# Kernel tuning notes

Hardware: AMD Instinct MI355X
Metric: run time of the kernel (lower is better)

The kernel has to match this reference:

```python
import jax, jax.numpy as jnp
import numpy as np

N, K, D, V = 20000, 16, 256, 64  # nodes, neighbors, embed_dim, edge vocab


def setup_inputs() -> dict:
    key = jax.random.key(0)
    ks = jax.random.split(key, 16)
    s = 1.0 / np.sqrt(2 * D)  # Linear(512 -> 256) init scale
    return {
        "node_reps": jax.random.normal(ks[0], (1, N, D), jnp.float32),
        "in_indices": jax.random.randint(ks[1], (1, N, K), 0, N, jnp.int32),
        "in_edges": jax.random.randint(ks[2], (1, N, K), 0, V, jnp.int32),
        "in_mask": jax.random.uniform(ks[3], (1, N, K), jnp.float32),
        "out_indices": jax.random.randint(ks[4], (1, N, K), 0, N, jnp.int32),
        "out_edges": jax.random.randint(ks[5], (1, N, K), 0, V, jnp.int32),
        "out_mask": jax.random.uniform(ks[6], (1, N, K), jnp.float32),
        "edge_emb_1": jax.random.normal(ks[7], (V, D), jnp.float32),
        "W_1": jax.random.uniform(ks[8], (2 * D, D), jnp.float32, -s, s),
        "b_1": jnp.zeros((D,), jnp.float32),
        "edge_emb_2": jax.random.normal(ks[9], (V, D), jnp.float32),
        "W_2": jax.random.uniform(ks[10], (2 * D, D), jnp.float32, -s, s),
        "b_2": jnp.zeros((D,), jnp.float32),
        "edge_emb_3": jax.random.normal(ks[11], (V, D), jnp.float32),
        "W_3": jax.random.uniform(ks[12], (2 * D, D), jnp.float32, -s, s),
        "b_3": jnp.zeros((D,), jnp.float32),
    }


def gcn_layer(node_reps, in_idx, in_edg, in_msk, out_idx, out_edg, out_msk,
              edge_emb, W, b):
    # node_reps: [1, N, D]; dropout is identity in eval mode.
    nodes = node_reps[0]  # [N, D]; batch_size == 1 as in the original repo

    def agg(idx, edg, msk):
        nbr = nodes[idx]          # gather: [1, N, K, D]
        erep = edge_emb[edg]      # embedding lookup: [1, N, K, D]
        reps = jnp.concatenate([nbr, erep], axis=3) * msk[..., None]
        return reps.sum(axis=2)   # masked sum over neighbors: [1, N, 2D]

    in_reps = agg(in_idx, in_edg, in_msk)
    out_reps = agg(out_idx, out_edg, out_msk)
    in_nodes = in_reps[0] @ W + b    # [N, D]
    out_nodes = out_reps[0] @ W + b  # [N, D]
    return node_reps + out_nodes + in_nodes  # broadcast -> [1, N, D]


def reference(node_reps, in_indices, in_edges, in_mask,
              out_indices, out_edges, out_mask,
              edge_emb_1, W_1, b_1, edge_emb_2, W_2, b_2, edge_emb_3, W_3, b_3):
    nbrs = (in_indices, in_edges, in_mask, out_indices, out_edges, out_mask)
    hidden = gcn_layer(node_reps, *nbrs, edge_emb_1, W_1, b_1)  # gc1
    mu = gcn_layer(hidden, *nbrs, edge_emb_2, W_2, b_2)          # gc2
    logvar = gcn_layer(hidden, *nbrs, edge_emb_3, W_3, b_3)      # gc3

    mu_t = jnp.tanh(mu[0])        # [N, D]
    lv_t = jnp.tanh(logvar[0])    # [N, D]
    n_nodes = mu_t.shape[0]
    kld = (-0.5 / n_nodes) * jnp.mean(
        jnp.sum(1.0 + 2.0 * lv_t - mu_t ** 2 - jnp.exp(lv_t) ** 2, axis=1))
    return hidden, kld
```

## Files before the change

kernel.cpp:

```cpp
#include <hip/hip_runtime.h>
#include <math.h>

#define NN 20000
#define KK 16
#define DD 256
#define VV 64
#define NT1 16

typedef __attribute__((ext_vector_type(8))) __bf16 bf16x8;
typedef __attribute__((ext_vector_type(4))) float floatx4;
typedef __attribute__((ext_vector_type(2))) float floatx2;
typedef __attribute__((ext_vector_type(8))) unsigned short ushort8;

__device__ __forceinline__ float4 ld4(const float* p) { return *reinterpret_cast<const float4*>(p); }

__device__ __forceinline__ unsigned short f2bf(float f) {
    union { float f; unsigned u; } v; v.f = f;
    unsigned r = v.u + 0x7FFFu + ((v.u >> 16) & 1u);
    return (unsigned short)(r >> 16);
}
__device__ __forceinline__ float bf2f(unsigned short u) {
    union { unsigned u; float f; } v; v.u = ((unsigned)u) << 16;
    return v.f;
}
__device__ __forceinline__ unsigned char f2q(float f) {
    return (unsigned char)(__builtin_amdgcn_cvt_pk_fp8_f32(f, 0.f, 0u, false) & 0xFFu);
}
__device__ __forceinline__ float q2f(unsigned char q) {
    floatx2 r = __builtin_amdgcn_cvt_pk_f32_fp8((unsigned)q, false);
    return r.x;
}
__device__ __forceinline__ float ftanh(float v) {
    float e = __expf(2.f * v);
    return 1.f - 2.f * __builtin_amdgcn_rcpf(e + 1.f);
}

__global__ __launch_bounds__(256) void ewk3(const float* __restrict__ e1, const float* __restrict__ W1,
                                            const float* __restrict__ e2, const float* __restrict__ W2,
                                            const float* __restrict__ e3, const float* __restrict__ W3,
                                            float* __restrict__ EW) {
    int layer = blockIdx.y;
    const float* emb = layer == 0 ? e1 : (layer == 1 ? e2 : e3);
    const float* W   = layer == 0 ? W1 : (layer == 1 ? W2 : W3);
    int v = blockIdx.x, d = threadIdx.x;
    float acc = 0.f;
    #pragma unroll 8
    for (int j = 0; j < 256; ++j)
        acc += emb[v * DD + j] * W[(size_t)(256 + j) * DD + d];
    EW[(size_t)layer * VV * DD + v * DD + d] = acc;
}

__global__ __launch_bounds__(256) void packU2(const float* __restrict__ W1, const float* __restrict__ EW1,
                                              const float* __restrict__ W2, const float* __restrict__ EW2,
                                              const float* __restrict__ W3, const float* __restrict__ EW3,
                                              unsigned short* __restrict__ U1, unsigned short* __restrict__ U23) {
    int blk = blockIdx.x;
    int NT; unsigned short* U; const float *Wa, *EWa, *Wb, *EWb; int g;
    if (blk < 40) { NT = 16; U = U1;  Wa = W1; EWa = EW1; Wb = W1; EWb = EW1; g = blk * 256 + threadIdx.x; }
    else          { NT = 32; U = U23; Wa = W2; EWa = EW2; Wb = W3; EWb = EW3; g = (blk - 40) * 256 + threadIdx.x; }
    int lane = g & 63, ntk = g >> 6;
    int nt = ntk % NT, kt = ntk / NT;
    if (kt >= 10) return;
    int n = nt * 16 + (lane & 15);
    int kbase = kt * 32 + (lane >> 4) * 8;
    const float* W = Wa; const float* EW = EWa;
    if (n >= 256) { W = Wb; EW = EWb; n -= 256; }
    unsigned short o8[8];
    #pragma unroll
    for (int j = 0; j < 8; ++j) {
        int k = kbase + j;
        float v = (k < 256) ? W[(size_t)k * DD + n] : EW[(size_t)(k - 256) * DD + n];
        o8[j] = f2bf(v);
    }
    *reinterpret_cast<uint4*>(&U[(size_t)g * 8]) = *reinterpret_cast<uint4*>(o8);
}

__global__ __launch_bounds__(256) void prep(const int* __restrict__ ie, const float* __restrict__ im,
                                            const int* __restrict__ oe, const float* __restrict__ om,
                                            const float* __restrict__ x,
                                            unsigned short* __restrict__ Hc, unsigned short* __restrict__ xh) {
    int w = threadIdx.x >> 6, lane = threadIdx.x & 63;
    int n = blockIdx.x * 4 + w;
    int e = 0; float m = 0.f;
    if (lane < 16)      { e = ie[n * KK + lane];      m = im[n * KK + lane]; }
    else if (lane < 32) { e = oe[n * KK + lane - 16]; m = om[n * KK + lane - 16]; }
    float h = 0.f;
    #pragma unroll
    for (int j = 0; j < 32; ++j) {
        int ev = __shfl(e, j);
        float mv = __shfl(m, j);
        if (ev == lane) h += mv;
    }
    Hc[(size_t)n * 64 + lane] = f2bf(h);
    size_t base = (size_t)blockIdx.x * 1024 + threadIdx.x * 4;
    float4 v = ld4(x + base);
    ushort4 o; o.x = f2bf(v.x); o.y = f2bf(v.y); o.z = f2bf(v.z); o.w = f2bf(v.w);
    *reinterpret_cast<ushort4*>(xh + base) = o;
}

__global__ __launch_bounds__(256) void fmm1(const unsigned short* __restrict__ xh, const unsigned short* __restrict__ Hc,
                                            const int* __restrict__ ii, const float* __restrict__ im,
                                            const int* __restrict__ oi, const float* __restrict__ om,
                                            const unsigned short* __restrict__ U, const float* __restrict__ b,
                                            float* __restrict__ out, unsigned char* __restrict__ h8) {
    __shared__ unsigned short sA[16 * 336];
    __shared__ int sidx[16][32];
    __shared__ float smsk[16][32];
    int n0 = blockIdx.x * 16;
    int tid = threadIdx.x;
    for (int q = tid; q < 512; q += 256) {
        int r = q >> 5, j = q & 31;
        int n = n0 + r;
        sidx[r][j] = (j < 16) ? ii[n * KK + j] : oi[n * KK + j - 16];
        smsk[r][j] = (j < 16) ? im[n * KK + j] : om[n * KK + j - 16];
    }
    if (tid < 128) {
        int r = tid >> 3, k8 = tid & 7;
        *reinterpret_cast<uint4*>(&sA[r * 336 + 256 + k8 * 8]) =
            *reinterpret_cast<const uint4*>(&Hc[(size_t)(n0 + r) * 64 + k8 * 8]);
    }
    __syncthreads();
    int lane = tid & 63, w = tid >> 6;
    int half = lane >> 5, c = (lane & 31) * 8;
    #pragma unroll
    for (int rr = 0; rr < 4; ++rr) {
        int row = w * 4 + rr;
        float acc[8] = {0.f, 0.f, 0.f, 0.f, 0.f, 0.f, 0.f, 0.f};
        #pragma unroll
        for (int j = 0; j < 16; ++j) {
            int j2 = j * 2 + half;
            int idx = sidx[row][j2];
            float m = smsk[row][j2];
            ushort8 u = *reinterpret_cast<const ushort8*>(xh + (size_t)idx * DD + c);
            #pragma unroll
            for (int z = 0; z < 8; ++z) acc[z] += m * bf2f(u[z]);
        }
        #pragma unroll
        for (int z = 0; z < 8; ++z) acc[z] += __shfl_xor(acc[z], 32);
        if (half == 0) {
            unsigned short o8[8];
            #pragma unroll
            for (int z = 0; z < 8; ++z) o8[z] = f2bf(acc[z]);
            *reinterpret_cast<uint4*>(&sA[row * 336 + c]) = *reinterpret_cast<uint4*>(o8);
        }
    }
    __syncthreads();
    int lr = lane & 15, quad = lane >> 4;
    float xp[4][4], bb[4];
    #pragma unroll
    for (int t = 0; t < 4; ++t) {
        int col = (w * 4 + t) * 16 + lr;
        bb[t] = 2.f * b[col];
        #pragma unroll
        for (int r = 0; r < 4; ++r)
            xp[t][r] = bf2f(xh[(size_t)(n0 + quad * 4 + r) * DD + col]);
    }
    floatx4 z = {0.f, 0.f, 0.f, 0.f};
    floatx4 acc[4] = {z, z, z, z};
    for (int kt = 0; kt < 10; ++kt) {
        bf16x8 a = *reinterpret_cast<const bf16x8*>(&sA[lr * 336 + kt * 32 + quad * 8]);
        #pragma unroll
        for (int t = 0; t < 4; ++t) {
            bf16x8 bf = *reinterpret_cast<const bf16x8*>(&U[(size_t)((kt * NT1 + w * 4 + t) * 64 + lane) * 8]);
            acc[t] = __builtin_amdgcn_mfma_f32_16x16x32_bf16(a, bf, acc[t], 0, 0, 0);
        }
    }
    #pragma unroll
    for (int t = 0; t < 4; ++t) {
        int col = (w * 4 + t) * 16 + lr;
        #pragma unroll
        for (int r = 0; r < 4; ++r) {
            size_t o = (size_t)(n0 + quad * 4 + r) * DD + col;
            float v = xp[t][r] + bb[t] + acc[t][r];
            out[o] = v;
            h8[o] = f2q(v);
        }
    }
}

__global__ __launch_bounds__(256) void fmm23(const unsigned char* __restrict__ h8, const unsigned short* __restrict__ Hc,
                                             const int* __restrict__ ii, const float* __restrict__ im,
                                             const int* __restrict__ oi, const float* __restrict__ om,
                                             const unsigned short* __restrict__ U, const float* __restrict__ b2,
                                             const float* __restrict__ b3, float* __restrict__ partials) {
    __shared__ unsigned short sA[16 * 336];
    __shared__ int sidx[16][32];
    __shared__ float smsk[16][32];
    __shared__ float red[4];
    int n0 = blockIdx.x * 16;
    int tid = threadIdx.x;
    for (int q = tid; q < 512; q += 256) {
        int r = q >> 5, j = q & 31;
        int n = n0 + r;
        sidx[r][j] = (j < 16) ? ii[n * KK + j] : oi[n * KK + j - 16];
        smsk[r][j] = (j < 16) ? im[n * KK + j] : om[n * KK + j - 16];
    }
    if (tid < 128) {
        int r = tid >> 3, k8 = tid & 7;
        *reinterpret_cast<uint4*>(&sA[r * 336 + 256 + k8 * 8]) =
            *reinterpret_cast<const uint4*>(&Hc[(size_t)(n0 + r) * 64 + k8 * 8]);
    }
    __syncthreads();
    int lane = tid & 63, w = tid >> 6;
    int g = lane >> 4, cl = lane & 15;
    #pragma unroll
    for (int rr = 0; rr < 4; ++rr) {
        int row = w * 4 + rr;
        float acc[16];
        #pragma unroll
        for (int z = 0; z < 16; ++z) acc[z] = 0.f;
        #pragma unroll
        for (int j = 0; j < 8; ++j) {
            int r = g * 8 + j;
            int idx = sidx[row][r];
            float m = smsk[row][r];
            uint4 u = *reinterpret_cast<const uint4*>(h8 + (size_t)idx * DD + cl * 16);
            unsigned dw[4] = {u.x, u.y, u.z, u.w};
            #pragma unroll
            for (int d = 0; d < 4; ++d) {
                floatx2 f01 = __builtin_amdgcn_cvt_pk_f32_fp8(dw[d], false);
                floatx2 f23 = __builtin_amdgcn_cvt_pk_f32_fp8(dw[d], true);
                acc[d * 4 + 0] += m * f01.x; acc[d * 4 + 1] += m * f01.y;
                acc[d * 4 + 2] += m * f23.x; acc[d * 4 + 3] += m * f23.y;
            }
        }
        #pragma unroll
        for (int z = 0; z < 16; ++z) {
            acc[z] += __shfl_xor(acc[z], 16);
            acc[z] += __shfl_xor(acc[z], 32);
        }
        if (g == 0) {
            unsigned short o16[16];
            #pragma unroll
            for (int z = 0; z < 16; ++z) o16[z] = f2bf(acc[z]);
            uint4* dst = reinterpret_cast<uint4*>(&sA[row * 336 + cl * 16]);
            dst[0] = reinterpret_cast<uint4*>(o16)[0];
            dst[1] = reinterpret_cast<uint4*>(o16)[1];
        }
    }
    __syncthreads();
    int lr = lane & 15, quad = lane >> 4;
    float hp[4][4], bm[4], bl[4];
    #pragma unroll
    for (int t = 0; t < 4; ++t) {
        int col = (w * 4 + t) * 16 + lr;
        bm[t] = 2.f * b2[col];
        bl[t] = 2.f * b3[col];
        #pragma unroll
        for (int r = 0; r < 4; ++r)
            hp[t][r] = q2f(h8[(size_t)(n0 + quad * 4 + r) * DD + col]);
    }
    floatx4 z = {0.f, 0.f, 0.f, 0.f};
    floatx4 am[4] = {z, z, z, z};
    floatx4 al[4] = {z, z, z, z};
    for (int kt = 0; kt < 10; ++kt) {
        bf16x8 a = *reinterpret_cast<const bf16x8*>(&sA[lr * 336 + kt * 32 + quad * 8]);
        #pragma unroll
        for (int t = 0; t < 4; ++t) {
            int nt = w * 4 + t;
            bf16x8 bmu = *reinterpret_cast<const bf16x8*>(&U[(size_t)((kt * 32 + nt) * 64 + lane) * 8]);
            bf16x8 blv = *reinterpret_cast<const bf16x8*>(&U[(size_t)((kt * 32 + 16 + nt) * 64 + lane) * 8]);
            am[t] = __builtin_amdgcn_mfma_f32_16x16x32_bf16(a, bmu, am[t], 0, 0, 0);
            al[t] = __builtin_amdgcn_mfma_f32_16x16x32_bf16(a, blv, al[t], 0, 0, 0);
        }
    }
    float kacc = 0.f;
    #pragma unroll
    for (int t = 0; t < 4; ++t) {
        #pragma unroll
        for (int r = 0; r < 4; ++r) {
            float h = hp[t][r];
            float tm = ftanh(h + bm[t] + am[t][r]);
            float tl = ftanh(h + bl[t] + al[t][r]);
            kacc += (1.f - tm * tm) + (2.f * tl - __expf(2.f * tl));
        }
    }
    #pragma unroll
    for (int off = 32; off > 0; off >>= 1) kacc += __shfl_xor(kacc, off);
    if (lane == 0) red[w] = kacc;
    __syncthreads();
    if (tid == 0)
        partials[blockIdx.x] = red[0] + red[1] + red[2] + red[3];
}

__global__ __launch_bounds__(256) void kred(const float* __restrict__ partials, int np,
                                            float* __restrict__ out) {
    __shared__ double red[256];
    double l = 0.0;
    for (int i = threadIdx.x; i < np; i += 256) l += (double)partials[i];
    red[threadIdx.x] = l;
    __syncthreads();
    for (int s = 128; s > 0; s >>= 1) {
        if (threadIdx.x < s) red[threadIdx.x] += red[threadIdx.x + s];
        __syncthreads();
    }
    if (threadIdx.x == 0)
        out[0] = (float)(red[0] * (-0.5 / ((double)NN * (double)NN)));
}

extern "C" void kernel_launch(void* const* d_in, const int* in_sizes, int n_in,
                              void* d_out, int out_size, void* d_ws, size_t ws_size,
                              hipStream_t stream) {
    const float* x  = (const float*)d_in[0];
    const int*   ii = (const int*)d_in[1];
    const int*   ie = (const int*)d_in[2];
    const float* im = (const float*)d_in[3];
    const int*   oi = (const int*)d_in[4];
    const int*   oe = (const int*)d_in[5];
    const float* om = (const float*)d_in[6];
    const float* e1 = (const float*)d_in[7];
    const float* W1 = (const float*)d_in[8];
    const float* b1 = (const float*)d_in[9];
    const float* e2 = (const float*)d_in[10];
    const float* W2 = (const float*)d_in[11];
    const float* b2 = (const float*)d_in[12];
    const float* e3 = (const float*)d_in[13];
    const float* W3 = (const float*)d_in[14];
    const float* b3 = (const float*)d_in[15];
    float* out = (float*)d_out;

    char* ws = (char*)d_ws;
    float*          EW    = (float*)(ws);
    unsigned short* U1    = (unsigned short*)(ws + 196608);
    unsigned short* U23   = (unsigned short*)(ws + 360448);
    float*          parts = (float*)(ws + 688128);
    unsigned short* Hc    = (unsigned short*)(ws + 696128);
    unsigned short* xh    = (unsigned short*)(ws + 3256128);
    unsigned char*  h8    = (unsigned char*)(ws + 13496128);

    ewk3  <<<dim3(VV, 3), 256, 0, stream>>>(e1, W1, e2, W2, e3, W3, EW);
    packU2<<<120, 256, 0, stream>>>(W1, EW, W2, EW + VV * DD, W3, EW + 2 * VV * DD, U1, U23);
    prep  <<<NN / 4, 256, 0, stream>>>(ie, im, oe, om, x, Hc, xh);
    fmm1  <<<NN / 16, 256, 0, stream>>>(xh, Hc, ii, im, oi, om, U1, b1, out, h8);
    fmm23 <<<NN / 16, 256, 0, stream>>>(h8, Hc, ii, im, oi, om, U23, b2, b3, parts);
    kred  <<<1, 256, 0, stream>>>(parts, NN / 16, out + (size_t)NN * DD);
}
```

Measured before the change: 223.8 us.

## Remap gather so each thread owns a row slice over all neighbors

Reorganizes the neighbor-gather phase in both fused kernels so each thread accumulates a 16-column slice of one node over all 32 neighbors. This removes the cross-lane shuffle reductions and the per-row loop. Residual and bias loads are hoisted before the gather to overlap their latency, the LDS row stride is padded from 336 to 352, and launch bounds request 4 blocks per CU. The trade-off is that each thread now issues more serial dependent loads (32 neighbors, unrolled by 8), and the occupancy hint may cap registers and cause spills.

After: 244.5 us. 1.09x slower.

```diff
diff --git a/kernel.cpp b/kernel.cpp
--- a/kernel.cpp
+++ b/kernel.cpp
@@ -6,6 +6,7 @@
 #define DD 256
 #define VV 64
 #define NT1 16
+#define SAS 352
 
 typedef __attribute__((ext_vector_type(8))) __bf16 bf16x8;
 typedef __attribute__((ext_vector_type(4))) float floatx4;
@@ -98,12 +99,12 @@
     *reinterpret_cast<ushort4*>(xh + base) = o;
 }
 
-__global__ __launch_bounds__(256) void fmm1(const unsigned short* __restrict__ xh, const unsigned short* __restrict__ Hc,
-                                            const int* __restrict__ ii, const float* __restrict__ im,
-                                            const int* __restrict__ oi, const float* __restrict__ om,
-                                            const unsigned short* __restrict__ U, const float* __restrict__ b,
-                                            float* __restrict__ out, unsigned char* __restrict__ h8) {
-    __shared__ unsigned short sA[16 * 336];
+__global__ __launch_bounds__(256, 4) void fmm1(const unsigned short* __restrict__ xh, const unsigned short* __restrict__ Hc,
+                                               const int* __restrict__ ii, const float* __restrict__ im,
+                                               const int* __restrict__ oi, const float* __restrict__ om,
+                                               const unsigned short* __restrict__ U, const float* __restrict__ b,
+                                               float* __restrict__ out, unsigned char* __restrict__ h8) {
+    __shared__ unsigned short sA[16 * SAS];
     __shared__ int sidx[16][32];
     __shared__ float smsk[16][32];
     int n0 = blockIdx.x * 16;
@@ -116,35 +117,10 @@
     }
     if (tid < 128) {
         int r = tid >> 3, k8 = tid & 7;
-        *reinterpret_cast<uint4*>(&sA[r * 336 + 256 + k8 * 8]) =
+        *reinterpret_cast<uint4*>(&sA[r * SAS + 256 + k8 * 8]) =
             *reinterpret_cast<const uint4*>(&Hc[(size_t)(n0 + r) * 64 + k8 * 8]);
     }
-    __syncthreads();
     int lane = tid & 63, w = tid >> 6;
-    int half = lane >> 5, c = (lane & 31) * 8;
-    #pragma unroll
-    for (int rr = 0; rr < 4; ++rr) {
-        int row = w * 4 + rr;
-        float acc[8] = {0.f, 0.f, 0.f, 0.f, 0.f, 0.f, 0.f, 0.f};
-        #pragma unroll
-        for (int j = 0; j < 16; ++j) {
-            int j2 = j * 2 + half;
-            int idx = sidx[row][j2];
-            float m = smsk[row][j2];
-            ushort8 u = *reinterpret_cast<const ushort8*>(xh + (size_t)idx * DD + c);
-            #pragma unroll
-            for (int z = 0; z < 8; ++z) acc[z] += m * bf2f(u[z]);
-        }
-        #pragma unroll
-        for (int z = 0; z < 8; ++z) acc[z] += __shfl_xor(acc[z], 32);
-        if (half == 0) {
-            unsigned short o8[8];
-            #pragma unroll
-            for (int z = 0; z < 8; ++z) o8[z] = f2bf(acc[z]);
-            *reinterpret_cast<uint4*>(&sA[row * 336 + c]) = *reinterpret_cast<uint4*>(o8);
-        }
-    }
-    __syncthreads();
     int lr = lane & 15, quad = lane >> 4;
     float xp[4][4], bb[4];
     #pragma unroll
@@ -155,10 +131,38 @@
         for (int r = 0; r < 4; ++r)
             xp[t][r] = bf2f(xh[(size_t)(n0 + quad * 4 + r) * DD + col]);
     }
+    __syncthreads();
+    {
+        int gr = tid >> 4, gc = tid & 15;
+        float acc[16];
+        #pragma unroll
+        for (int z = 0; z < 16; ++z) acc[z] = 0.f;
+        const unsigned short* basecol = xh + gc * 16;
+        #pragma unroll 8
+        for (int j = 0; j < 32; ++j) {
+            int idx = sidx[gr][j];
+            float m = smsk[gr][j];
+            const unsigned short* p = basecol + (size_t)idx * DD;
+            ushort8 u0 = *reinterpret_cast<const ushort8*>(p);
+            ushort8 u1 = *reinterpret_cast<const ushort8*>(p + 8);
+            #pragma unroll
+            for (int z = 0; z < 8; ++z) {
+                acc[z]     += m * bf2f(u0[z]);
+                acc[z + 8] += m * bf2f(u1[z]);
+            }
+        }
+        unsigned short o16[16];
+        #pragma unroll
+        for (int z = 0; z < 16; ++z) o16[z] = f2bf(acc[z]);
+        uint4* dst = reinterpret_cast<uint4*>(&sA[gr * SAS + gc * 16]);
+        dst[0] = reinterpret_cast<uint4*>(o16)[0];
+        dst[1] = reinterpret_cast<uint4*>(o16)[1];
+    }
+    __syncthreads();
     floatx4 z = {0.f, 0.f, 0.f, 0.f};
     floatx4 acc[4] = {z, z, z, z};
     for (int kt = 0; kt < 10; ++kt) {
-        bf16x8 a = *reinterpret_cast<const bf16x8*>(&sA[lr * 336 + kt * 32 + quad * 8]);
+        bf16x8 a = *reinterpret_cast<const bf16x8*>(&sA[lr * SAS + kt * 32 + quad * 8]);
         #pragma unroll
         for (int t = 0; t < 4; ++t) {
             bf16x8 bf = *reinterpret_cast<const bf16x8*>(&U[(size_t)((kt * NT1 + w * 4 + t) * 64 + lane) * 8]);
@@ -178,12 +182,12 @@
     }
 }
 
-__global__ __launch_bounds__(256) void fmm23(const unsigned char* __restrict__ h8, const unsigned short* __restrict__ Hc,
-                                             const int* __restrict__ ii, const float* __restrict__ im,
-                                             const int* __restrict__ oi, const float* __restrict__ om,
-                                             const unsigned short* __restrict__ U, const float* __restrict__ b2,
-                                             const float* __restrict__ b3, float* __restrict__ partials) {
-    __shared__ unsigned short sA[16 * 336];
+__global__ __launch_bounds__(256, 4) void fmm23(const unsigned char* __restrict__ h8, const unsigned short* __restrict__ Hc,
+                                                const int* __restrict__ ii, const float* __restrict__ im,
+                                                const int* __restrict__ oi, const float* __restrict__ om,
+                                                const unsigned short* __restrict__ U, const float* __restrict__ b2,
+                                                const float* __restrict__ b3, float* __restrict__ partials) {
+    __shared__ unsigned short sA[16 * SAS];
     __shared__ int sidx[16][32];
     __shared__ float smsk[16][32];
     __shared__ float red[4];
@@ -197,24 +201,33 @@
     }
     if (tid < 128) {
         int r = tid >> 3, k8 = tid & 7;
-        *reinterpret_cast<uint4*>(&sA[r * 336 + 256 + k8 * 8]) =
+        *reinterpret_cast<uint4*>(&sA[r * SAS + 256 + k8 * 8]) =
             *reinterpret_cast<const uint4*>(&Hc[(size_t)(n0 + r) * 64 + k8 * 8]);
     }
-    __syncthreads();
     int lane = tid & 63, w = tid >> 6;
-    int g = lane >> 4, cl = lane & 15;
-    #pragma unroll
-    for (int rr = 0; rr < 4; ++rr) {
-        int row = w * 4 + rr;
+    int lr = lane & 15, quad = lane >> 4;
+    float hp[4][4], bm[4], bl[4];
+    #pragma unroll
+    for (int t = 0; t < 4; ++t) {
+        int col = (w * 4 + t) * 16 + lr;
+        bm[t] = 2.f * b2[col];
+        bl[t] = 2.f * b3[col];
+        #pragma unroll
+        for (int r = 0; r < 4; ++r)
+            hp[t][r] = q2f(h8[(size_t)(n0 + quad * 4 + r) * DD + col]);
+    }
+    __syncthreads();
+    {
+        int gr = tid >> 4, gc = tid & 15;
         float acc[16];
         #pragma unroll
         for (int z = 0; z < 16; ++z) acc[z] = 0.f;
-        #pragma unroll
-        for (int j = 0; j < 8; ++j) {
-            int r = g * 8 + j;
-            int idx = sidx[row][r];
-            float m = smsk[row][r];
-            uint4 u = *reinterpret_cast<const uint4*>(h8 + (size_t)idx * DD + cl * 16);
+        const unsigned char* basecol = h8 + gc * 16;
+        #pragma unroll 8
+        for (int j = 0; j < 32; ++j) {
+            int idx = sidx[gr][j];
+            float m = smsk[gr][j];
+            uint4 u = *reinterpret_cast<const uint4*>(basecol + (size_t)idx * DD);
             unsigned dw[4] = {u.x, u.y, u.z, u.w};
             #pragma unroll
             for (int d = 0; d < 4; ++d) {
@@ -224,37 +237,19 @@
                 acc[d * 4 + 2] += m * f23.x; acc[d * 4 + 3] += m * f23.y;
             }
         }
-        #pragma unroll
-        for (int z = 0; z < 16; ++z) {
-            acc[z] += __shfl_xor(acc[z], 16);
-            acc[z] += __shfl_xor(acc[z], 32);
-        }
-        if (g == 0) {
-            unsigned short o16[16];
-            #pragma unroll
-            for (int z = 0; z < 16; ++z) o16[z] = f2bf(acc[z]);
-            uint4* dst = reinterpret_cast<uint4*>(&sA[row * 336 + cl * 16]);
-            dst[0] = reinterpret_cast<uint4*>(o16)[0];
-            dst[1] = reinterpret_cast<uint4*>(o16)[1];
-        }
-    }
-    __syncthreads();
-    int lr = lane & 15, quad = lane >> 4;
-    float hp[4][4], bm[4], bl[4];
-    #pragma unroll
-    for (int t = 0; t < 4; ++t) {
-        int col = (w * 4 + t) * 16 + lr;
-        bm[t] = 2.f * b2[col];
-        bl[t] = 2.f * b3[col];
-        #pragma unroll
-        for (int r = 0; r < 4; ++r)
-            hp[t][r] = q2f(h8[(size_t)(n0 + quad * 4 + r) * DD + col]);
-    }
+        unsigned short o16[16];
+        #pragma unroll
+        for (int z = 0; z < 16; ++z) o16[z] = f2bf(acc[z]);
+        uint4* dst = reinterpret_cast<uint4*>(&sA[gr * SAS + gc * 16]);
+        dst[0] = reinterpret_cast<uint4*>(o16)[0];
+        dst[1] = reinterpret_cast<uint4*>(o16)[1];
+    }
+    __syncthreads();
     floatx4 z = {0.f, 0.f, 0.f, 0.f};
     floatx4 am[4] = {z, z, z, z};
     floatx4 al[4] = {z, z, z, z};
     for (int kt = 0; kt < 10; ++kt) {
-        bf16x8 a = *reinterpret_cast<const bf16x8*>(&sA[lr * 336 + kt * 32 + quad * 8]);
+        bf16x8 a = *reinterpret_cast<const bf16x8*>(&sA[lr * SAS + kt * 32 + quad * 8]);
         #pragma unroll
         for (int t = 0; t < 4; ++t) {
             int nt = w * 4 + t;
```

## Fuse setup kernels, switch layers 2/3 matmul to FP8 MFMA, atomic KLD reduction

Applied to the files above, without the earlier changes.

Merges the edge-embedding projection, weight packing and prep into one setup launch, computing the EW rows inline inside the packing threads. Layers 2 and 3 now store weights, edge histograms and the aggregated A tile in FP8 and use the fp8 MFMA, which halves operand bytes and LDS traffic. The separate reduction kernel is replaced by a memset plus per-block float atomicAdd. This cuts launch count and memory traffic, but lowers numerical precision, makes the KLD sum order nondeterministic, and the fused EW computation is redundant across threads.

New measurement: 202.0 us. -9.7%, faster.

```diff
diff --git a/kernel.cpp b/kernel.cpp
--- a/kernel.cpp
+++ b/kernel.cpp
@@ -6,6 +6,8 @@
 #define DD 256
 #define VV 64
 #define NT1 16
+#define SAS 336
+#define SAS8 336
 
 typedef __attribute__((ext_vector_type(8))) __bf16 bf16x8;
 typedef __attribute__((ext_vector_type(4))) float floatx4;
@@ -35,67 +37,77 @@
     return 1.f - 2.f * __builtin_amdgcn_rcpf(e + 1.f);
 }
 
-__global__ __launch_bounds__(256) void ewk3(const float* __restrict__ e1, const float* __restrict__ W1,
-                                            const float* __restrict__ e2, const float* __restrict__ W2,
-                                            const float* __restrict__ e3, const float* __restrict__ W3,
-                                            float* __restrict__ EW) {
-    int layer = blockIdx.y;
-    const float* emb = layer == 0 ? e1 : (layer == 1 ? e2 : e3);
-    const float* W   = layer == 0 ? W1 : (layer == 1 ? W2 : W3);
-    int v = blockIdx.x, d = threadIdx.x;
-    float acc = 0.f;
-    #pragma unroll 8
-    for (int j = 0; j < 256; ++j)
-        acc += emb[v * DD + j] * W[(size_t)(256 + j) * DD + d];
-    EW[(size_t)layer * VV * DD + v * DD + d] = acc;
-}
-
-__global__ __launch_bounds__(256) void packU2(const float* __restrict__ W1, const float* __restrict__ EW1,
-                                              const float* __restrict__ W2, const float* __restrict__ EW2,
-                                              const float* __restrict__ W3, const float* __restrict__ EW3,
-                                              unsigned short* __restrict__ U1, unsigned short* __restrict__ U23) {
-    int blk = blockIdx.x;
-    int NT; unsigned short* U; const float *Wa, *EWa, *Wb, *EWb; int g;
-    if (blk < 40) { NT = 16; U = U1;  Wa = W1; EWa = EW1; Wb = W1; EWb = EW1; g = blk * 256 + threadIdx.x; }
-    else          { NT = 32; U = U23; Wa = W2; EWa = EW2; Wb = W3; EWb = EW3; g = (blk - 40) * 256 + threadIdx.x; }
-    int lane = g & 63, ntk = g >> 6;
-    int nt = ntk % NT, kt = ntk / NT;
-    if (kt >= 10) return;
-    int n = nt * 16 + (lane & 15);
-    int kbase = kt * 32 + (lane >> 4) * 8;
-    const float* W = Wa; const float* EW = EWa;
-    if (n >= 256) { W = Wb; EW = EWb; n -= 256; }
-    unsigned short o8[8];
-    #pragma unroll
-    for (int j = 0; j < 8; ++j) {
-        int k = kbase + j;
-        float v = (k < 256) ? W[(size_t)k * DD + n] : EW[(size_t)(k - 256) * DD + n];
-        o8[j] = f2bf(v);
-    }
-    *reinterpret_cast<uint4*>(&U[(size_t)g * 8]) = *reinterpret_cast<uint4*>(o8);
-}
-
-__global__ __launch_bounds__(256) void prep(const int* __restrict__ ie, const float* __restrict__ im,
-                                            const int* __restrict__ oe, const float* __restrict__ om,
-                                            const float* __restrict__ x,
-                                            unsigned short* __restrict__ Hc, unsigned short* __restrict__ xh) {
-    int w = threadIdx.x >> 6, lane = threadIdx.x & 63;
-    int n = blockIdx.x * 4 + w;
-    int e = 0; float m = 0.f;
-    if (lane < 16)      { e = ie[n * KK + lane];      m = im[n * KK + lane]; }
-    else if (lane < 32) { e = oe[n * KK + lane - 16]; m = om[n * KK + lane - 16]; }
-    float h = 0.f;
-    #pragma unroll
-    for (int j = 0; j < 32; ++j) {
-        int ev = __shfl(e, j);
-        float mv = __shfl(m, j);
-        if (ev == lane) h += mv;
-    }
-    Hc[(size_t)n * 64 + lane] = f2bf(h);
-    size_t base = (size_t)blockIdx.x * 1024 + threadIdx.x * 4;
-    float4 v = ld4(x + base);
-    ushort4 o; o.x = f2bf(v.x); o.y = f2bf(v.y); o.z = f2bf(v.z); o.w = f2bf(v.w);
-    *reinterpret_cast<ushort4*>(xh + base) = o;
+__global__ __launch_bounds__(256) void setup(
+    const int* __restrict__ ie, const float* __restrict__ im,
+    const int* __restrict__ oe, const float* __restrict__ om,
+    const float* __restrict__ x,
+    const float* __restrict__ e1, const float* __restrict__ W1,
+    const float* __restrict__ e2, const float* __restrict__ W2,
+    const float* __restrict__ e3, const float* __restrict__ W3,
+    unsigned short* __restrict__ U1, unsigned char* __restrict__ U23,
+    unsigned short* __restrict__ Hc, unsigned char* __restrict__ Hc8,
+    unsigned short* __restrict__ xh) {
+    int blk = blockIdx.x, tid = threadIdx.x;
+    if (blk < 120) {
+        int u1path = blk < 40;
+        int NT = u1path ? 16 : 32;
+        int g = (u1path ? blk : blk - 40) * 256 + tid;
+        int lane = g & 63, ntk = g >> 6;
+        int nt = ntk % NT, kt = ntk / NT;
+        if (kt >= 10) return;
+        int n = nt * 16 + (lane & 15);
+        int kbase = kt * 32 + (lane >> 4) * 8;
+        const float* W; const float* emb;
+        if (u1path)       { W = W1; emb = e1; }
+        else if (n < 256) { W = W2; emb = e2; }
+        else              { W = W3; emb = e3; n -= 256; }
+        float vals[8];
+        if (kbase < 256) {
+            #pragma unroll
+            for (int j = 0; j < 8; ++j) vals[j] = W[(size_t)(kbase + j) * DD + n];
+        } else {
+            int vb = kbase - 256;
+            #pragma unroll
+            for (int z = 0; z < 8; ++z) vals[z] = 0.f;
+            #pragma unroll 4
+            for (int j = 0; j < 256; ++j) {
+                float wv = W[(size_t)(256 + j) * DD + n];
+                #pragma unroll
+                for (int z = 0; z < 8; ++z) vals[z] += emb[(vb + z) * DD + j] * wv;
+            }
+        }
+        if (u1path) {
+            unsigned short o8[8];
+            #pragma unroll
+            for (int j = 0; j < 8; ++j) o8[j] = f2bf(vals[j]);
+            *reinterpret_cast<uint4*>(&U1[(size_t)g * 8]) = *reinterpret_cast<uint4*>(o8);
+        } else {
+            unsigned char o8[8];
+            #pragma unroll
+            for (int j = 0; j < 8; ++j) o8[j] = f2q(vals[j]);
+            *reinterpret_cast<uint2*>(&U23[(size_t)g * 8]) = *reinterpret_cast<uint2*>(o8);
+        }
+    } else {
+        int pb = blk - 120;
+        int w = tid >> 6, lane = tid & 63;
+        int n = pb * 4 + w;
+        int e = 0; float m = 0.f;
+        if (lane < 16)      { e = ie[n * KK + lane];      m = im[n * KK + lane]; }
+        else if (lane < 32) { e = oe[n * KK + lane - 16]; m = om[n * KK + lane - 16]; }
+        float h = 0.f;
+        #pragma unroll
+        for (int j = 0; j < 32; ++j) {
+            int ev = __shfl(e, j);
+            float mv = __shfl(m, j);
+            if (ev == lane) h += mv;
+        }
+        Hc [(size_t)n * 64 + lane] = f2bf(h);
+        Hc8[(size_t)n * 64 + lane] = f2q(h);
+        size_t base = (size_t)pb * 1024 + tid * 4;
+        float4 v = ld4(x + base);
+        ushort4 o; o.x = f2bf(v.x); o.y = f2bf(v.y); o.z = f2bf(v.z); o.w = f2bf(v.w);
+        *reinterpret_cast<ushort4*>(xh + base) = o;
+    }
 }
 
 __global__ __launch_bounds__(256) void fmm1(const unsigned short* __restrict__ xh, const unsigned short* __restrict__ Hc,
@@ -103,7 +115,7 @@
                                             const int* __restrict__ oi, const float* __restrict__ om,
                                             const unsigned short* __restrict__ U, const float* __restrict__ b,
                                             float* __restrict__ out, unsigned char* __restrict__ h8) {
-    __shared__ unsigned short sA[16 * 336];
+    __shared__ unsigned short sA[16 * SAS];
     __shared__ int sidx[16][32];
     __shared__ float smsk[16][32];
     int n0 = blockIdx.x * 16;
@@ -116,7 +128,7 @@
     }
     if (tid < 128) {
         int r = tid >> 3, k8 = tid & 7;
-        *reinterpret_cast<uint4*>(&sA[r * 336 + 256 + k8 * 8]) =
+        *reinterpret_cast<uint4*>(&sA[r * SAS + 256 + k8 * 8]) =
             *reinterpret_cast<const uint4*>(&Hc[(size_t)(n0 + r) * 64 + k8 * 8]);
     }
     __syncthreads();
@@ -141,7 +153,7 @@
             unsigned short o8[8];
             #pragma unroll
             for (int z = 0; z < 8; ++z) o8[z] = f2bf(acc[z]);
-            *reinterpret_cast<uint4*>(&sA[row * 336 + c]) = *reinterpret_cast<uint4*>(o8);
+            *reinterpret_cast<uint4*>(&sA[row * SAS + c]) = *reinterpret_cast<uint4*>(o8);
         }
     }
     __syncthreads();
@@ -158,7 +170,7 @@
     floatx4 z = {0.f, 0.f, 0.f, 0.f};
     floatx4 acc[4] = {z, z, z, z};
     for (int kt = 0; kt < 10; ++kt) {
-        bf16x8 a = *reinterpret_cast<const bf16x8*>(&sA[lr * 336 + kt * 32 + quad * 8]);
+        bf16x8 a = *reinterpret_cast<const bf16x8*>(&sA[lr * SAS + kt * 32 + quad * 8]);
         #pragma unroll
         for (int t = 0; t < 4; ++t) {
             bf16x8 bf = *reinterpret_cast<const bf16x8*>(&U[(size_t)((kt * NT1 + w * 4 + t) * 64 + lane) * 8]);
@@ -178,12 +190,12 @@
     }
 }
 
-__global__ __launch_bounds__(256) void fmm23(const unsigned char* __restrict__ h8, const unsigned short* __restrict__ Hc,
+__global__ __launch_bounds__(256) void fmm23(const unsigned char* __restrict__ h8, const unsigned char* __restrict__ Hc8,
                                              const int* __restrict__ ii, const float* __restrict__ im,
                                              const int* __restrict__ oi, const float* __restrict__ om,
-                                             const unsigned short* __restrict__ U, const float* __restrict__ b2,
-                                             const float* __restrict__ b3, float* __restrict__ partials) {
-    __shared__ unsigned short sA[16 * 336];
+                                             const unsigned char* __restrict__ U, const float* __restrict__ b2,
+                                             const float* __restrict__ b3, float* __restrict__ kld) {
+    __shared__ unsigned char sA[16 * SAS8];
     __shared__ int sidx[16][32];
     __shared__ float smsk[16][32];
     __shared__ float red[4];
@@ -197,8 +209,8 @@
     }
     if (tid < 128) {
         int r = tid >> 3, k8 = tid & 7;
-        *reinterpret_cast<uint4*>(&sA[r * 336 + 256 + k8 * 8]) =
-            *reinterpret_cast<const uint4*>(&Hc[(size_t)(n0 + r) * 64 + k8 * 8]);
+        *reinterpret_cast<uint2*>(&sA[r * SAS8 + 256 + k8 * 8]) =
+            *reinterpret_cast<const uint2*>(&Hc8[(size_t)(n0 + r) * 64 + k8 * 8]);
     }
     __syncthreads();
     int lane = tid & 63, w = tid >> 6;
@@ -230,12 +242,10 @@
             acc[z] += __shfl_xor(acc[z], 32);
         }
         if (g == 0) {
-            unsigned short o16[16];
-            #pragma unroll
-            for (int z = 0; z < 16; ++z) o16[z] = f2bf(acc[z]);
-            uint4* dst = reinterpret_cast<uint4*>(&sA[row * 336 + cl * 16]);
-            dst[0] = reinterpret_cast<uint4*>(o16)[0];
-            dst[1] = reinterpret_cast<uint4*>(o16)[1];
+            unsigned char o16[16];
+            #pragma unroll
+            for (int z = 0; z < 16; ++z) o16[z] = f2q(acc[z]);
+            *reinterpret_cast<uint4*>(&sA[row * SAS8 + cl * 16]) = *reinterpret_cast<uint4*>(o16);
         }
     }
     __syncthreads();
@@ -254,14 +264,14 @@
     floatx4 am[4] = {z, z, z, z};
     floatx4 al[4] = {z, z, z, z};
     for (int kt = 0; kt < 10; ++kt) {
-        bf16x8 a = *reinterpret_cast<const bf16x8*>(&sA[lr * 336 + kt * 32 + quad * 8]);
+        long a = *reinterpret_cast<const long*>(&sA[lr * SAS8 + kt * 32 + quad * 8]);
         #pragma unroll
         for (int t = 0; t < 4; ++t) {
             int nt = w * 4 + t;
-            bf16x8 bmu = *reinterpret_cast<const bf16x8*>(&U[(size_t)((kt * 32 + nt) * 64 + lane) * 8]);
-            bf16x8 blv = *reinterpret_cast<const bf16x8*>(&U[(size_t)((kt * 32 + 16 + nt) * 64 + lane) * 8]);
-            am[t] = __builtin_amdgcn_mfma_f32_16x16x32_bf16(a, bmu, am[t], 0, 0, 0);
-            al[t] = __builtin_amdgcn_mfma_f32_16x16x32_bf16(a, blv, al[t], 0, 0, 0);
+            long bmu = *reinterpret_cast<const long*>(&U[(size_t)((kt * 32 + nt) * 64 + lane) * 8]);
+            long blv = *reinterpret_cast<const long*>(&U[(size_t)((kt * 32 + 16 + nt) * 64 + lane) * 8]);
+            am[t] = __builtin_amdgcn_mfma_f32_16x16x32_fp8_fp8(a, bmu, am[t], 0, 0, 0);
+            al[t] = __builtin_amdgcn_mfma_f32_16x16x32_fp8_fp8(a, blv, al[t], 0, 0, 0);
         }
     }
     float kacc = 0.f;
@@ -280,22 +290,7 @@
     if (lane == 0) red[w] = kacc;
     __syncthreads();
     if (tid == 0)
-        partials[blockIdx.x] = red[0] + red[1] + red[2] + red[3];
-}
-
-__global__ __launch_bounds__(256) void kred(const float* __restrict__ partials, int np,
-                                            float* __restrict__ out) {
-    __shared__ double red[256];
-    double l = 0.0;
-    for (int i = threadIdx.x; i < np; i += 256) l += (double)partials[i];
-    red[threadIdx.x] = l;
-    __syncthreads();
-    for (int s = 128; s > 0; s >>= 1) {
-        if (threadIdx.x < s) red[threadIdx.x] += red[threadIdx.x + s];
-        __syncthreads();
-    }
-    if (threadIdx.x == 0)
-        out[0] = (float)(red[0] * (-0.5 / ((double)NN * (double)NN)));
+        atomicAdd(kld, (red[0] + red[1] + red[2] + red[3]) * (-0.5f / ((float)NN * (float)NN)));
 }
 
 extern "C" void kernel_launch(void* const* d_in, const int* in_sizes, int n_in,
@@ -320,18 +315,17 @@
     float* out = (float*)d_out;
 
     char* ws = (char*)d_ws;
-    float*          EW    = (float*)(ws);
-    unsigned short* U1    = (unsigned short*)(ws + 196608);
-    unsigned short* U23   = (unsigned short*)(ws + 360448);
-    float*          parts = (float*)(ws + 688128);
-    unsigned short* Hc    = (unsigned short*)(ws + 696128);
-    unsigned short* xh    = (unsigned short*)(ws + 3256128);
-    unsigned char*  h8    = (unsigned char*)(ws + 13496128);
-
-    ewk3  <<<dim3(VV, 3), 256, 0, stream>>>(e1, W1, e2, W2, e3, W3, EW);
-    packU2<<<120, 256, 0, stream>>>(W1, EW, W2, EW + VV * DD, W3, EW + 2 * VV * DD, U1, U23);
-    prep  <<<NN / 4, 256, 0, stream>>>(ie, im, oe, om, x, Hc, xh);
-    fmm1  <<<NN / 16, 256, 0, stream>>>(xh, Hc, ii, im, oi, om, U1, b1, out, h8);
-    fmm23 <<<NN / 16, 256, 0, stream>>>(h8, Hc, ii, im, oi, om, U23, b2, b3, parts);
-    kred  <<<1, 256, 0, stream>>>(parts, NN / 16, out + (size_t)NN * DD);
-}
+    unsigned short* U1  = (unsigned short*)(ws);
+    unsigned char*  U23 = (unsigned char*)(ws + 163840);
+    unsigned short* Hc  = (unsigned short*)(ws + 327680);
+    unsigned char*  Hc8 = (unsigned char*)(ws + 2887680);
+    unsigned short* xh  = (unsigned short*)(ws + 4167680);
+    unsigned char*  h8  = (unsigned char*)(ws + 14407680);
+
+    hipMemsetAsync(out + (size_t)NN * DD, 0, 4, stream);
+    setup<<<120 + NN / 4, 256, 0, stream>>>(ie, im, oe, om, x, e1, W1, e2, W2, e3, W3,
+                                            U1, U23, Hc, Hc8, xh);
+    fmm1 <<<NN / 16, 256, 0, stream>>>(xh, Hc, ii, im, oi, om, U1, b1, out, h8);
+    fmm23<<<NN / 16, 256, 0, stream>>>(h8, Hc8, ii, im, oi, om, U23, b2, b3,
+                                       out + (size_t)NN * DD);
+}
```
